# Kernel tuning notes

Measured on AMD Instinct MI355X. Metric: run time of the kernel, lower is better.

## Reference

```python
import jax, jax.numpy as jnp
import numpy as np

N = 50000      # nodes
E = 800000     # edges
G = 512        # graphs in batch
F0 = 92        # orig atom feature len
F = 64         # atom_fea_len
NB = 41        # nbr_fea_len
H = 128        # h_fea_len
NCONV = 3
EPS = 1e-5


def setup_inputs() -> dict:
    key = jax.random.key(0)
    ks = jax.random.split(key, 16)
    s = 0.05
    inp = {
        "x": jax.random.normal(ks[0], (N, F0), jnp.float32),
        "edge_index": jax.random.randint(ks[1], (2, E), 0, N),
        "edge_attr": jax.random.normal(ks[2], (E, NB), jnp.float32),
        "batch": jnp.sort(jax.random.randint(ks[3], (N,), 0, G)),
        # embedding (only applied at the first conv, when x width == F0)
        "emb_W": jax.random.normal(ks[4], (F0, F), jnp.float32) * s,
        "emb_b": jnp.zeros((F,), jnp.float32),
        # per-conv-layer params, stacked on leading axis
        "bn1_g": jnp.ones((NCONV, F), jnp.float32),
        "bn1_b": jnp.zeros((NCONV, F), jnp.float32),
        "bn2_g": jnp.ones((NCONV, F), jnp.float32),
        "bn2_b": jnp.zeros((NCONV, F), jnp.float32),
        "lnf_W": jax.random.normal(ks[5], (NCONV, 2 * F + NB, F), jnp.float32) * s,
        "lnf_b": jnp.zeros((NCONV, F), jnp.float32),
        "lns_W": jax.random.normal(ks[6], (NCONV, 2 * F + NB, F), jnp.float32) * s,
        "lns_b": jnp.zeros((NCONV, F), jnp.float32),
        # readout MLP
        "fc1_W": jax.random.normal(ks[7], (F, H), jnp.float32) * s,
        "fc1_b": jnp.zeros((H,), jnp.float32),
        "out_W": jax.random.normal(ks[8], (H, 1), jnp.float32) * s,
        "out_b": jnp.zeros((1,), jnp.float32),
    }
    return inp


def _batchnorm(x, g, b):
    # training-mode BatchNorm1d: batch stats over node dim, biased variance
    mean = jnp.mean(x, axis=0)
    var = jnp.var(x, axis=0)
    return (x - mean) * jax.lax.rsqrt(var + EPS) * g + b


def _cgconv(x, edge_index, edge_attr, bn1_g, bn1_b, bn2_g, bn2_b, Wf, bf, Ws, bs):
    x = _batchnorm(x, bn1_g, bn1_b)
    # flow='target_to_source': x_i = x[edge_index[0]], x_j = x[edge_index[1]],
    # aggregation scatter-adds messages to edge_index[0]
    src, dst = edge_index[0], edge_index[1]
    z = jnp.concatenate([x[src], x[dst], edge_attr], axis=-1)   # [E, 2F+NB]
    m = jax.nn.sigmoid(z @ Wf + bf) * jax.nn.softplus(z @ Ws + bs)
    agg = jax.ops.segment_sum(m, src, num_segments=x.shape[0])  # [N, F]
    out = _batchnorm(agg, bn2_g, bn2_b) + x
    return jax.nn.softplus(out)


def reference(x, edge_index, edge_attr, batch, emb_W, emb_b,
              bn1_g, bn1_b, bn2_g, bn2_b, lnf_W, lnf_b, lns_W, lns_b,
              fc1_W, fc1_b, out_W, out_b):
    h = x @ emb_W + emb_b  # first conv applies embedding (x width == F0)
    for i in range(NCONV):
        h = _cgconv(h, edge_index, edge_attr,
                    bn1_g[i], bn1_b[i], bn2_g[i], bn2_b[i],
                    lnf_W[i], lnf_b[i], lns_W[i], lns_b[i])
    # global mean pool per graph
    sums = jax.ops.segment_sum(h, batch, num_segments=G)
    cnts = jax.ops.segment_sum(jnp.ones((h.shape[0], 1), h.dtype), batch, num_segments=G)
    crys = sums / jnp.maximum(cnts, 1.0)                         # [G, F]
    crys = jax.nn.softplus(jax.nn.softplus(crys) @ fc1_W + fc1_b)
    return crys @ out_W + out_b                                  # [G, 1]
```

## Files before the change

### kernel.cpp

```cpp
#include <hip/hip_runtime.h>
#include <hip/hip_bf16.h>

#define NN 50000
#define NE 800000
#define NG 512
#define F0 92
#define FF 64
#define NB 41
#define HH 128
#define NBLK_SCAN 196
#define NBATCH (NE / 64)
#define WBSZ (2 * 8 * 64 * 8)

typedef __attribute__((ext_vector_type(4))) float f32x4;
typedef __attribute__((ext_vector_type(8))) short bf16x8;

__device__ __forceinline__ float softplusf(float x) {
    return fmaxf(x, 0.f) + __logf(1.f + __expf(-fabsf(x)));
}
__device__ __forceinline__ float sigmoidf(float x) {
    return __fdividef(1.f, 1.f + __expf(-x));
}
__device__ __forceinline__ ushort f2bf(float v) {
    __hip_bfloat16 b = __float2bfloat16(v);
    return *reinterpret_cast<ushort*>(&b);
}


__global__ __launch_bounds__(256) void hist_kernel(const int* __restrict__ ei,
                                                   int* __restrict__ cnt)
{
    for (int e = blockIdx.x * 256 + threadIdx.x; e < NE; e += gridDim.x * 256)
        atomicAdd(&cnt[ei[e]], 1);
}

__global__ __launch_bounds__(256) void scan1_kernel(const int* __restrict__ cnt,
                                                    int* __restrict__ bsum)
{
    __shared__ int sd[256];
    const int t = threadIdx.x;
    const int idx = blockIdx.x * 256 + t;
    sd[t] = (idx < NN) ? cnt[idx] : 0;
    __syncthreads();
    for (int s = 128; s > 0; s >>= 1) {
        if (t < s) sd[t] += sd[t + s];
        __syncthreads();
    }
    if (t == 0) bsum[blockIdx.x] = sd[0];
}

__global__ __launch_bounds__(256) void scan2_kernel(int* __restrict__ bsum)
{
    __shared__ int sd[256];
    const int t = threadIdx.x;
    const int v = (t < NBLK_SCAN) ? bsum[t] : 0;
    sd[t] = v;
    __syncthreads();
    for (int off = 1; off < 256; off <<= 1) {
        int a = (t >= off) ? sd[t - off] : 0;
        __syncthreads();
        sd[t] += a;
        __syncthreads();
    }
    if (t < NBLK_SCAN) bsum[t] = sd[t] - v;
}

__global__ __launch_bounds__(256) void scan3_kernel(const int* __restrict__ cnt,
                                                    const int* __restrict__ bsum,
                                                    int* __restrict__ cursor)
{
    __shared__ int sd[256];
    const int t = threadIdx.x;
    const int idx = blockIdx.x * 256 + t;
    const int v = (idx < NN) ? cnt[idx] : 0;
    sd[t] = v;
    __syncthreads();
    for (int off = 1; off < 256; off <<= 1) {
        int a = (t >= off) ? sd[t - off] : 0;
        __syncthreads();
        sd[t] += a;
        __syncthreads();
    }
    if (idx < NN) cursor[idx] = bsum[blockIdx.x] + sd[t] - v;
}

__global__ __launch_bounds__(256) void scatter_kernel(const int* __restrict__ ei,
                                                      int* __restrict__ cursor,
                                                      int4* __restrict__ esd)
{
    for (int e = blockIdx.x * 256 + threadIdx.x; e < NE; e += gridDim.x * 256) {
        const int s = ei[e];
        const int d = ei[NE + e];
        const int pos = atomicAdd(&cursor[s], 1);
        esd[pos] = make_int4(e, s, d, 0);
    }
}

__global__ __launch_bounds__(256) void pack_kernel(const float* __restrict__ ea,
                                                   const int4* __restrict__ esd,
                                                   ushort* __restrict__ eaP)
{
    const int pos = blockIdx.x * 256 + threadIdx.x;
    if (pos >= NE) return;
    const int e = esd[pos].x;
    const float* row = ea + (size_t)e * NB;
    const int gg = pos >> 4, rw = pos & 15;
#pragma unroll
    for (int t2 = 0; t2 < 2; ++t2)
#pragma unroll
        for (int lg = 0; lg < 4; ++lg) {
            ushort buf[8] __attribute__((aligned(16)));
#pragma unroll
            for (int j = 0; j < 8; ++j) {
                const int k = t2 * 32 + lg * 8 + j;
                buf[j] = (k < NB) ? f2bf(row[k]) : (ushort)0;
            }
            *(int4*)&eaP[(((size_t)gg * 2 + t2) * 64 + lg * 16 + rw) * 8] =
                *(const int4*)buf;
        }
}

__global__ __launch_bounds__(256) void prep_kernel(
    const float* __restrict__ lnfW, const float* __restrict__ lnsW,
    ushort* __restrict__ wB)
{
    const int total = 3 * WBSZ;
    for (int idx = blockIdx.x * 256 + threadIdx.x; idx < total; idx += gridDim.x * 256) {
        const int j = idx & 7;
        const int lane = (idx >> 3) & 63;
        const int nt = (idx >> 9) & 7;
        const int t2 = (idx >> 12) & 1;
        const int i = idx >> 13;
        const int k = t2 * 32 + (lane >> 4) * 8 + j;
        const int col = (nt & 3) * 16 + (lane & 15);
        const float* W = (nt < 4 ? lnfW : lnsW) + (size_t)i * 169 * FF;
        wB[idx] = (k < NB) ? f2bf(W[(2 * FF + k) * FF + col]) : (ushort)0;
    }
}


__global__ __launch_bounds__(256) void emb_kernel(
    const float* __restrict__ x, const float* __restrict__ W,
    const float* __restrict__ bias, float* __restrict__ h,
    float* __restrict__ stats0)
{
    __shared__ float sx[4][F0];
    __shared__ float sdr[2][4][FF];
    const int lane = threadIdx.x & 63;
    const int w = threadIdx.x >> 6;
    float wr[F0];
#pragma unroll
    for (int k = 0; k < F0; ++k) wr[k] = W[k * FF + lane];
    const float bv = bias[lane];
    float s = 0.f, s2 = 0.f;
    const int nit = NN / 4;
    for (int it = blockIdx.x; it < nit; it += gridDim.x) {
        const int n = it * 4 + w;
        if (lane < 46) {
            sx[w][lane * 2]     = x[n * F0 + lane * 2];
            sx[w][lane * 2 + 1] = x[n * F0 + lane * 2 + 1];
        }
        __syncthreads();
        float acc = bv;
#pragma unroll
        for (int k4 = 0; k4 < F0 / 4; ++k4) {
            float4 q = *(const float4*)&sx[w][k4 * 4];
            acc = fmaf(q.x, wr[k4 * 4 + 0], acc);
            acc = fmaf(q.y, wr[k4 * 4 + 1], acc);
            acc = fmaf(q.z, wr[k4 * 4 + 2], acc);
            acc = fmaf(q.w, wr[k4 * 4 + 3], acc);
        }
        h[n * FF + lane] = acc;
        s += acc;
        s2 = fmaf(acc, acc, s2);
        __syncthreads();
    }
    sdr[0][w][lane] = s;
    sdr[1][w][lane] = s2;
    __syncthreads();
    if (threadIdx.x < FF) {
        const int f = threadIdx.x;
        atomicAdd(&stats0[f],      sdr[0][0][f] + sdr[0][1][f] + sdr[0][2][f] + sdr[0][3][f]);
        atomicAdd(&stats0[FF + f], sdr[1][0][f] + sdr[1][1][f] + sdr[1][2][f] + sdr[1][3][f]);
    }
}

__global__ __launch_bounds__(256) void stats_kernel(
    const float* __restrict__ src, float* __restrict__ stats)
{
    __shared__ float sd[2][4][FF];
    const int f = threadIdx.x & 63;
    const int r = threadIdx.x >> 6;
    float s = 0.f, s2 = 0.f;
    for (int n = blockIdx.x * 4 + r; n < NN; n += gridDim.x * 4) {
        float v = src[n * FF + f];
        s += v;
        s2 = fmaf(v, v, s2);
    }
    sd[0][r][f] = s;
    sd[1][r][f] = s2;
    __syncthreads();
    if (threadIdx.x < FF) {
        atomicAdd(&stats[f],      sd[0][0][f] + sd[0][1][f] + sd[0][2][f] + sd[0][3][f]);
        atomicAdd(&stats[FF + f], sd[1][0][f] + sd[1][1][f] + sd[1][2][f] + sd[1][3][f]);
    }
}

__global__ void finalize_kernel(const float* __restrict__ g, const float* __restrict__ b,
                                float* __restrict__ stats)
{
    const int f = threadIdx.x;
    const float inv = 1.f / (float)NN;
    float mean = stats[f] * inv;
    float var = stats[FF + f] * inv - mean * mean;
    float rstd = rsqrtf(var + 1e-5f);
    float A = rstd * g[f];
    stats[2 * FF + f] = A;
    stats[3 * FF + f] = fmaf(-mean, A, b[f]);
}

__global__ __launch_bounds__(256) void node_kernel(
    const float* __restrict__ h, const float* __restrict__ stats,
    const float* __restrict__ Wf, const float* __restrict__ Ws,
    const float* __restrict__ bf, const float* __restrict__ bs,
    float* __restrict__ xn, float* __restrict__ pS, float* __restrict__ pD)
{
    __shared__ float sx[4][FF];
    const int lane = threadIdx.x & 63;
    const int w = threadIdx.x >> 6;
    const float* W = (w < 2) ? Wf : Ws;
    const int rowbase = (w & 1) * FF;
    float wr[FF];
#pragma unroll
    for (int k = 0; k < FF; ++k) wr[k] = W[(rowbase + k) * FF + lane];
    const float A = stats[2 * FF + lane];
    const float B = stats[3 * FF + lane];
    float bias = 0.f;
    if (w == 0) bias = bf[lane];
    if (w == 2) bias = bs[lane];
    float* outp = ((w & 1) ? pD : pS) + ((w >> 1) & 1);
    for (int n = blockIdx.x; n < NN; n += gridDim.x) {
        const float xv = fmaf(h[n * FF + lane], A, B);
        if (w == 0) xn[n * FF + lane] = xv;
        sx[w][lane] = xv;
        __syncthreads();
        float acc = bias;
#pragma unroll
        for (int k4 = 0; k4 < FF / 4; ++k4) {
            float4 q = *(const float4*)&sx[w][k4 * 4];
            acc = fmaf(q.x, wr[k4 * 4 + 0], acc);
            acc = fmaf(q.y, wr[k4 * 4 + 1], acc);
            acc = fmaf(q.z, wr[k4 * 4 + 2], acc);
            acc = fmaf(q.w, wr[k4 * 4 + 3], acc);
        }
        outp[(size_t)n * 128 + 2 * lane] = acc;
        __syncthreads();
    }
}

__global__ __launch_bounds__(256) __attribute__((amdgpu_waves_per_eu(4, 4)))
void edge_kernel(const ushort* __restrict__ eaP, const int4* __restrict__ esd,
                 const ushort* __restrict__ wB,
                 const float* __restrict__ pS, const float* __restrict__ pD,
                 float* __restrict__ agg)
{
    __shared__ ushort wlds[WBSZ];
    __shared__ float  mld[4][64 * 17 + 4];
    __shared__ int    sld[4][64];
    __shared__ int    dld[4][64];
    const int t = threadIdx.x, lane = t & 63, w = t >> 6;
    for (int i = t; i < WBSZ / 8; i += 256)
        ((int4*)wlds)[i] = ((const int4*)wB)[i];
    __syncthreads();
    const int le = lane >> 4, lf = lane & 15;
    const int nw = (gridDim.x * 256) >> 6;
    const int gw = (blockIdx.x * 256 + t) >> 6;

    for (int b = gw; b < NBATCH; b += nw) {
        const int pos = b * 64 + lane;
        const int4 rec = esd[pos];
        sld[w][lane] = rec.y;
        dld[w][lane] = rec.z;
        bf16x8 af[4][2];
#pragma unroll
        for (int g = 0; g < 4; ++g)
#pragma unroll
            for (int t2 = 0; t2 < 2; ++t2)
                af[g][t2] = *(const bf16x8*)&eaP[(((size_t)(b * 4 + g) * 2 + t2) * 64 + lane) * 8];

#pragma unroll
        for (int p = 0; p < 4; ++p) {
            const bf16x8 bG0 = *(const bf16x8*)&wlds[((0 * 8 + p) * 64 + lane) * 8];
            const bf16x8 bG1 = *(const bf16x8*)&wlds[((1 * 8 + p) * 64 + lane) * 8];
            const bf16x8 bC0 = *(const bf16x8*)&wlds[((0 * 8 + p + 4) * 64 + lane) * 8];
            const bf16x8 bC1 = *(const bf16x8*)&wlds[((1 * 8 + p + 4) * 64 + lane) * 8];
            const int f = p * 16 + lf;
#pragma unroll
            for (int g = 0; g < 4; ++g) {
                f32x4 aG = {0.f, 0.f, 0.f, 0.f}, aC = {0.f, 0.f, 0.f, 0.f};
                aG = __builtin_amdgcn_mfma_f32_16x16x32_bf16(af[g][0], bG0, aG, 0, 0, 0);
                aG = __builtin_amdgcn_mfma_f32_16x16x32_bf16(af[g][1], bG1, aG, 0, 0, 0);
                aC = __builtin_amdgcn_mfma_f32_16x16x32_bf16(af[g][0], bC0, aC, 0, 0, 0);
                aC = __builtin_amdgcn_mfma_f32_16x16x32_bf16(af[g][1], bC1, aC, 0, 0, 0);
                const int eb = g * 16 + le * 4;
#pragma unroll
                for (int r = 0; r < 4; ++r) {
                    const int eidx = eb + r;
                    const int sv = sld[w][eidx];
                    const int dv = dld[w][eidx];
                    const float2 s2 = *(const float2*)(pS + (size_t)sv * 128 + 2 * f);
                    const float2 d2 = *(const float2*)(pD + (size_t)dv * 128 + 2 * f);
                    mld[w][eidx * 17 + lf] =
                        sigmoidf(aG[r] + s2.x + d2.x) * softplusf(aC[r] + s2.y + d2.y);
                }
            }
            const int f0 = p * 16;
            for (int s = 0; s < 16; ++s) {
                const int eidx = s * 4 + le;
                float v = mld[w][eidx * 17 + lf];
                const int sA = sld[w][eidx];
                const int sB = (le <= 2) ? sld[w][eidx + 1] : -1;
                const int sC = (le <= 1) ? sld[w][eidx + 2] : -1;
                const float t1 = __shfl_down(v, 16, 64);
                if (sB == sA) v += t1;
                const float t2v = __shfl_down(v, 32, 64);
                if (sC == sA) v += t2v;
                const bool head = (le == 0) || (sld[w][eidx - 1] != sA);
                if (head) unsafeAtomicAdd(&agg[(size_t)sA * FF + f0 + lf], v);
            }
        }
    }
}

__global__ __launch_bounds__(256) void update_kernel(
    const float* __restrict__ agg, const float* __restrict__ xn,
    const float* __restrict__ stats, float* __restrict__ h,
    const int* __restrict__ batch, float* __restrict__ pool,
    float* __restrict__ pcnt, float* __restrict__ statsNext, const int do_pool)
{
    __shared__ float sdr[2][4][FF];
    float s = 0.f, s2 = 0.f;
    const int total = NN * FF;
    for (int idx = blockIdx.x * blockDim.x + threadIdx.x; idx < total;
         idx += gridDim.x * blockDim.x) {
        const int f = idx & 63;
        const int n = idx >> 6;
        const float A = stats[2 * FF + f];
        const float B = stats[3 * FF + f];
        const float v = softplusf(fmaf(agg[idx], A, B) + xn[idx]);
        if (do_pool) {
            const int g = batch[n];
            unsafeAtomicAdd(&pool[g * FF + f], v);
            if (f == 0) unsafeAtomicAdd(&pcnt[g], 1.f);
        } else {
            h[idx] = v;
            s += v;
            s2 = fmaf(v, v, s2);
        }
    }
    if (!do_pool) {
        const int f = threadIdx.x & 63, r = threadIdx.x >> 6;
        sdr[0][r][f] = s;
        sdr[1][r][f] = s2;
        __syncthreads();
        if (threadIdx.x < FF) {
            atomicAdd(&statsNext[f],      sdr[0][0][f] + sdr[0][1][f] + sdr[0][2][f] + sdr[0][3][f]);
            atomicAdd(&statsNext[FF + f], sdr[1][0][f] + sdr[1][1][f] + sdr[1][2][f] + sdr[1][3][f]);
        }
    }
}

__global__ __launch_bounds__(128) void readout_kernel(
    const float* __restrict__ pool, const float* __restrict__ pcnt,
    const float* __restrict__ fc1W, const float* __restrict__ fc1b,
    const float* __restrict__ outW, const float* __restrict__ outb,
    float* __restrict__ out)
{
    __shared__ float sp[FF];
    __shared__ float red[2];
    const int g = blockIdx.x;
    const int t = threadIdx.x;
    if (t < FF) {
        const float c = fmaxf(pcnt[g], 1.f);
        sp[t] = softplusf(pool[g * FF + t] / c);
    }
    __syncthreads();
    float a = fc1b[t];
#pragma unroll
    for (int k = 0; k < FF; ++k) a = fmaf(sp[k], fc1W[k * HH + t], a);
    float o = softplusf(a) * outW[t];
#pragma unroll
    for (int off = 32; off > 0; off >>= 1) o += __shfl_down(o, off, 64);
    if ((t & 63) == 0) red[t >> 6] = o;
    __syncthreads();
    if (t == 0) out[g] = red[0] + red[1] + outb[0];
}

extern "C" void kernel_launch(void* const* d_in, const int* in_sizes, int n_in,
                              void* d_out, int out_size, void* d_ws, size_t ws_size,
                              hipStream_t stream)
{
    const float* x     = (const float*)d_in[0];
    const int*   ei    = (const int*)  d_in[1];
    const float* ea    = (const float*)d_in[2];
    const int*   batch = (const int*)  d_in[3];
    const float* embW  = (const float*)d_in[4];
    const float* embb  = (const float*)d_in[5];
    const float* bn1g  = (const float*)d_in[6];
    const float* bn1b  = (const float*)d_in[7];
    const float* bn2g  = (const float*)d_in[8];
    const float* bn2b  = (const float*)d_in[9];
    const float* lnfW  = (const float*)d_in[10];
    const float* lnfb  = (const float*)d_in[11];
    const float* lnsW  = (const float*)d_in[12];
    const float* lnsb  = (const float*)d_in[13];
    const float* fc1W  = (const float*)d_in[14];
    const float* fc1b  = (const float*)d_in[15];
    const float* outW  = (const float*)d_in[16];
    const float* outb  = (const float*)d_in[17];

    float* ws      = (float*)d_ws;
    float* h       = ws;
    float* xn      = h   + (size_t)NN * FF;
    float* pS      = xn  + (size_t)NN * FF;
    float* pD      = pS  + (size_t)NN * 128;
    float* agg     = pD  + (size_t)NN * 128;
    float* pool    = agg + (size_t)NN * FF;
    float* pcnt    = pool + (size_t)NG * FF;
    float* statsB1 = pcnt + NG;
    float* statsB2 = statsB1 + 3 * 256;
    int*   cnt     = (int*)(statsB2 + 3 * 256);
    int*   cursor  = cnt + NN;
    int*   bsum    = cursor + NN;
    int4*  esd     = (int4*)(bsum + 256);
    ushort* wB     = (ushort*)(esd + NE);
    ushort* eaP    = wB + 3 * WBSZ;

    hipMemsetAsync(cnt, 0, NN * sizeof(int), stream);
    hipMemsetAsync(pool, 0, (NG * FF + NG + 6 * 256) * sizeof(float), stream);

    hist_kernel<<<2048, 256, 0, stream>>>(ei, cnt);
    scan1_kernel<<<NBLK_SCAN, 256, 0, stream>>>(cnt, bsum);
    scan2_kernel<<<1, 256, 0, stream>>>(bsum);
    scan3_kernel<<<NBLK_SCAN, 256, 0, stream>>>(cnt, bsum, cursor);
    scatter_kernel<<<2048, 256, 0, stream>>>(ei, cursor, esd);
    pack_kernel<<<(NE + 255) / 256, 256, 0, stream>>>(ea, esd, eaP);
    prep_kernel<<<96, 256, 0, stream>>>(lnfW, lnsW, wB);
    emb_kernel<<<1024, 256, 0, stream>>>(x, embW, embb, h, statsB1);

    for (int i = 0; i < 3; ++i) {
        const float* Wf  = lnfW + (size_t)i * 169 * FF;
        const float* Wsp = lnsW + (size_t)i * 169 * FF;
        float* s1 = statsB1 + (size_t)i * 256;
        float* s2 = statsB2 + (size_t)i * 256;
        finalize_kernel<<<1, 64, 0, stream>>>(bn1g + i * FF, bn1b + i * FF, s1);
        node_kernel<<<1024, 256, 0, stream>>>(h, s1, Wf, Wsp,
                                              lnfb + i * FF, lnsb + i * FF, xn, pS, pD);
        hipMemsetAsync(agg, 0, (size_t)NN * FF * sizeof(float), stream);
        edge_kernel<<<1024, 256, 0, stream>>>(eaP, esd, wB + (size_t)i * WBSZ,
                                              pS, pD, agg);
        stats_kernel<<<256, 256, 0, stream>>>(agg, s2);
        finalize_kernel<<<1, 64, 0, stream>>>(bn2g + i * FF, bn2b + i * FF, s2);
        update_kernel<<<2048, 256, 0, stream>>>(agg, xn, s2, h, batch, pool, pcnt,
                                                statsB1 + (size_t)(i + 1 < 3 ? i + 1 : 0) * 256,
                                                (i == 2) ? 1 : 0);
    }
    readout_kernel<<<NG, HH, 0, stream>>>(pool, pcnt, fc1W, fc1b, outW, outb, (float*)d_out);
}
```

Before: 948.6 us.

## Pack edge features in original order, gather per edge in edge kernel, fold BN finalize

The pack kernel now converts edge attributes to bf16 in original edge order, staging rows through shared memory, so it no longer does a sorted-order indirect gather. The edge kernel instead gathers each edge's packed row by its original id, obtained with lane shuffles. It also drops the LDS staging of messages and the segmented reduction, replacing them with a per-lane running sum over 4 consecutive sorted edges and atomics at segment breaks. The BN finalize kernels are folded into node_kernel and update_kernel, and the edge grid is doubled with the waves_per_eu hint removed. The trade-offs are random gathers of edge features, more global atomics per edge, and unroll-1 loops that may limit latency hiding.

After: 1.057 ms. 1.11x slower.

```diff
diff --git a/kernel.cpp b/kernel.cpp
--- a/kernel.cpp
+++ b/kernel.cpp
@@ -11,6 +11,7 @@
 #define NBLK_SCAN 196
 #define NBATCH (NE / 64)
 #define WBSZ (2 * 8 * 64 * 8)
+#define PACK_EB 128
 
 typedef __attribute__((ext_vector_type(4))) float f32x4;
 typedef __attribute__((ext_vector_type(8))) short bf16x8;
@@ -96,28 +97,24 @@
     }
 }
 
-__global__ __launch_bounds__(256) void pack_kernel(const float* __restrict__ ea,
-                                                   const int4* __restrict__ esd,
+__global__ __launch_bounds__(128) void pack_kernel(const float* __restrict__ ea,
                                                    ushort* __restrict__ eaP)
 {
-    const int pos = blockIdx.x * 256 + threadIdx.x;
-    if (pos >= NE) return;
-    const int e = esd[pos].x;
-    const float* row = ea + (size_t)e * NB;
-    const int gg = pos >> 4, rw = pos & 15;
-#pragma unroll
-    for (int t2 = 0; t2 < 2; ++t2)
-#pragma unroll
-        for (int lg = 0; lg < 4; ++lg) {
-            ushort buf[8] __attribute__((aligned(16)));
-#pragma unroll
-            for (int j = 0; j < 8; ++j) {
-                const int k = t2 * 32 + lg * 8 + j;
-                buf[j] = (k < NB) ? f2bf(row[k]) : (ushort)0;
-            }
-            *(int4*)&eaP[(((size_t)gg * 2 + t2) * 64 + lg * 16 + rw) * 8] =
-                *(const int4*)buf;
-        }
+    __shared__ float rowbuf[PACK_EB * NB];
+    const int t = threadIdx.x;
+    const size_t base = (size_t)blockIdx.x * PACK_EB;
+    const float* src = ea + base * NB;
+    for (int i = t; i < PACK_EB * NB; i += 128) rowbuf[i] = src[i];
+    __syncthreads();
+    uint* out = (uint*)eaP + base * 32;
+#pragma unroll
+    for (int i = 0; i < 32; ++i) {
+        const int idx = i * 128 + t;
+        const int e = idx >> 5, k2 = (idx & 31) * 2;
+        const float v0 = (k2 < NB) ? rowbuf[e * NB + k2] : 0.f;
+        const float v1 = (k2 + 1 < NB) ? rowbuf[e * NB + k2 + 1] : 0.f;
+        out[idx] = (uint)f2bf(v0) | ((uint)f2bf(v1) << 16);
+    }
 }
 
 __global__ __launch_bounds__(256) void prep_kernel(
@@ -206,21 +203,9 @@
     }
 }
 
-__global__ void finalize_kernel(const float* __restrict__ g, const float* __restrict__ b,
-                                float* __restrict__ stats)
-{
-    const int f = threadIdx.x;
-    const float inv = 1.f / (float)NN;
-    float mean = stats[f] * inv;
-    float var = stats[FF + f] * inv - mean * mean;
-    float rstd = rsqrtf(var + 1e-5f);
-    float A = rstd * g[f];
-    stats[2 * FF + f] = A;
-    stats[3 * FF + f] = fmaf(-mean, A, b[f]);
-}
-
 __global__ __launch_bounds__(256) void node_kernel(
     const float* __restrict__ h, const float* __restrict__ stats,
+    const float* __restrict__ gbn, const float* __restrict__ bbn,
     const float* __restrict__ Wf, const float* __restrict__ Ws,
     const float* __restrict__ bf, const float* __restrict__ bs,
     float* __restrict__ xn, float* __restrict__ pS, float* __restrict__ pD)
@@ -233,8 +218,11 @@
     float wr[FF];
 #pragma unroll
     for (int k = 0; k < FF; ++k) wr[k] = W[(rowbase + k) * FF + lane];
-    const float A = stats[2 * FF + lane];
-    const float B = stats[3 * FF + lane];
+    const float inv = 1.f / (float)NN;
+    const float mean = stats[lane] * inv;
+    const float var = stats[FF + lane] * inv - mean * mean;
+    const float A = rsqrtf(var + 1e-5f) * gbn[lane];
+    const float B = fmaf(-mean, A, bbn[lane]);
     float bias = 0.f;
     if (w == 0) bias = bf[lane];
     if (w == 2) bias = bs[lane];
@@ -258,17 +246,14 @@
     }
 }
 
-__global__ __launch_bounds__(256) __attribute__((amdgpu_waves_per_eu(4, 4)))
+__global__ __launch_bounds__(256)
 void edge_kernel(const ushort* __restrict__ eaP, const int4* __restrict__ esd,
                  const ushort* __restrict__ wB,
                  const float* __restrict__ pS, const float* __restrict__ pD,
                  float* __restrict__ agg)
 {
     __shared__ ushort wlds[WBSZ];
-    __shared__ float  mld[4][64 * 17 + 4];
-    __shared__ int    sld[4][64];
-    __shared__ int    dld[4][64];
-    const int t = threadIdx.x, lane = t & 63, w = t >> 6;
+    const int t = threadIdx.x, lane = t & 63;
     for (int i = t; i < WBSZ / 8; i += 256)
         ((int4*)wlds)[i] = ((const int4*)wB)[i];
     __syncthreads();
@@ -277,56 +262,53 @@
     const int gw = (blockIdx.x * 256 + t) >> 6;
 
     for (int b = gw; b < NBATCH; b += nw) {
-        const int pos = b * 64 + lane;
-        const int4 rec = esd[pos];
-        sld[w][lane] = rec.y;
-        dld[w][lane] = rec.z;
-        bf16x8 af[4][2];
-#pragma unroll
-        for (int g = 0; g < 4; ++g)
-#pragma unroll
-            for (int t2 = 0; t2 < 2; ++t2)
-                af[g][t2] = *(const bf16x8*)&eaP[(((size_t)(b * 4 + g) * 2 + t2) * 64 + lane) * 8];
-
-#pragma unroll
-        for (int p = 0; p < 4; ++p) {
-            const bf16x8 bG0 = *(const bf16x8*)&wlds[((0 * 8 + p) * 64 + lane) * 8];
-            const bf16x8 bG1 = *(const bf16x8*)&wlds[((1 * 8 + p) * 64 + lane) * 8];
-            const bf16x8 bC0 = *(const bf16x8*)&wlds[((0 * 8 + p + 4) * 64 + lane) * 8];
-            const bf16x8 bC1 = *(const bf16x8*)&wlds[((1 * 8 + p + 4) * 64 + lane) * 8];
-            const int f = p * 16 + lf;
-#pragma unroll
-            for (int g = 0; g < 4; ++g) {
+        const int4 rec = esd[b * 64 + lane];
+#pragma unroll 1
+        for (int g = 0; g < 4; ++g) {
+            const int eg  = __shfl(rec.x, g * 16 + lf, 64);
+            const int sv0 = __shfl(rec.y, g * 16 + le * 4 + 0, 64);
+            const int sv1 = __shfl(rec.y, g * 16 + le * 4 + 1, 64);
+            const int sv2 = __shfl(rec.y, g * 16 + le * 4 + 2, 64);
+            const int sv3 = __shfl(rec.y, g * 16 + le * 4 + 3, 64);
+            const int dv0 = __shfl(rec.z, g * 16 + le * 4 + 0, 64);
+            const int dv1 = __shfl(rec.z, g * 16 + le * 4 + 1, 64);
+            const int dv2 = __shfl(rec.z, g * 16 + le * 4 + 2, 64);
+            const int dv3 = __shfl(rec.z, g * 16 + le * 4 + 3, 64);
+            const bf16x8 af0 = *(const bf16x8*)&eaP[(size_t)eg * 64 + le * 8];
+            const bf16x8 af1 = *(const bf16x8*)&eaP[(size_t)eg * 64 + 32 + le * 8];
+#pragma unroll 1
+            for (int p = 0; p < 4; ++p) {
+                const bf16x8 bG0 = *(const bf16x8*)&wlds[((0 * 8 + p) * 64 + lane) * 8];
+                const bf16x8 bG1 = *(const bf16x8*)&wlds[((1 * 8 + p) * 64 + lane) * 8];
+                const bf16x8 bC0 = *(const bf16x8*)&wlds[((0 * 8 + p + 4) * 64 + lane) * 8];
+                const bf16x8 bC1 = *(const bf16x8*)&wlds[((1 * 8 + p + 4) * 64 + lane) * 8];
                 f32x4 aG = {0.f, 0.f, 0.f, 0.f}, aC = {0.f, 0.f, 0.f, 0.f};
-                aG = __builtin_amdgcn_mfma_f32_16x16x32_bf16(af[g][0], bG0, aG, 0, 0, 0);
-                aG = __builtin_amdgcn_mfma_f32_16x16x32_bf16(af[g][1], bG1, aG, 0, 0, 0);
-                aC = __builtin_amdgcn_mfma_f32_16x16x32_bf16(af[g][0], bC0, aC, 0, 0, 0);
-                aC = __builtin_amdgcn_mfma_f32_16x16x32_bf16(af[g][1], bC1, aC, 0, 0, 0);
-                const int eb = g * 16 + le * 4;
-#pragma unroll
-                for (int r = 0; r < 4; ++r) {
-                    const int eidx = eb + r;
-                    const int sv = sld[w][eidx];
-                    const int dv = dld[w][eidx];
-                    const float2 s2 = *(const float2*)(pS + (size_t)sv * 128 + 2 * f);
-                    const float2 d2 = *(const float2*)(pD + (size_t)dv * 128 + 2 * f);
-                    mld[w][eidx * 17 + lf] =
-                        sigmoidf(aG[r] + s2.x + d2.x) * softplusf(aC[r] + s2.y + d2.y);
-                }
-            }
-            const int f0 = p * 16;
-            for (int s = 0; s < 16; ++s) {
-                const int eidx = s * 4 + le;
-                float v = mld[w][eidx * 17 + lf];
-                const int sA = sld[w][eidx];
-                const int sB = (le <= 2) ? sld[w][eidx + 1] : -1;
-                const int sC = (le <= 1) ? sld[w][eidx + 2] : -1;
-                const float t1 = __shfl_down(v, 16, 64);
-                if (sB == sA) v += t1;
-                const float t2v = __shfl_down(v, 32, 64);
-                if (sC == sA) v += t2v;
-                const bool head = (le == 0) || (sld[w][eidx - 1] != sA);
-                if (head) unsafeAtomicAdd(&agg[(size_t)sA * FF + f0 + lf], v);
+                aG = __builtin_amdgcn_mfma_f32_16x16x32_bf16(af0, bG0, aG, 0, 0, 0);
+                aG = __builtin_amdgcn_mfma_f32_16x16x32_bf16(af1, bG1, aG, 0, 0, 0);
+                aC = __builtin_amdgcn_mfma_f32_16x16x32_bf16(af0, bC0, aC, 0, 0, 0);
+                aC = __builtin_amdgcn_mfma_f32_16x16x32_bf16(af1, bC1, aC, 0, 0, 0);
+                const int fo = 2 * (p * 16 + lf);
+                const float2 s20 = *(const float2*)(pS + (size_t)sv0 * 128 + fo);
+                const float2 d20 = *(const float2*)(pD + (size_t)dv0 * 128 + fo);
+                const float2 s21 = *(const float2*)(pS + (size_t)sv1 * 128 + fo);
+                const float2 d21 = *(const float2*)(pD + (size_t)dv1 * 128 + fo);
+                const float2 s22 = *(const float2*)(pS + (size_t)sv2 * 128 + fo);
+                const float2 d22 = *(const float2*)(pD + (size_t)dv2 * 128 + fo);
+                const float2 s23 = *(const float2*)(pS + (size_t)sv3 * 128 + fo);
+                const float2 d23 = *(const float2*)(pD + (size_t)dv3 * 128 + fo);
+                const float m0 = sigmoidf(aG[0] + s20.x + d20.x) * softplusf(aC[0] + s20.y + d20.y);
+                const float m1 = sigmoidf(aG[1] + s21.x + d21.x) * softplusf(aC[1] + s21.y + d21.y);
+                const float m2 = sigmoidf(aG[2] + s22.x + d22.x) * softplusf(aC[2] + s22.y + d22.y);
+                const float m3 = sigmoidf(aG[3] + s23.x + d23.x) * softplusf(aC[3] + s23.y + d23.y);
+                const int fcol = p * 16 + lf;
+                float run = m0;
+                if (sv1 == sv0) run += m1;
+                else { unsafeAtomicAdd(&agg[(size_t)sv0 * FF + fcol], run); run = m1; }
+                if (sv2 == sv1) run += m2;
+                else { unsafeAtomicAdd(&agg[(size_t)sv1 * FF + fcol], run); run = m2; }
+                if (sv3 == sv2) run += m3;
+                else { unsafeAtomicAdd(&agg[(size_t)sv2 * FF + fcol], run); run = m3; }
+                unsafeAtomicAdd(&agg[(size_t)sv3 * FF + fcol], run);
             }
         }
     }
@@ -334,24 +316,29 @@
 
 __global__ __launch_bounds__(256) void update_kernel(
     const float* __restrict__ agg, const float* __restrict__ xn,
-    const float* __restrict__ stats, float* __restrict__ h,
-    const int* __restrict__ batch, float* __restrict__ pool,
-    float* __restrict__ pcnt, float* __restrict__ statsNext, const int do_pool)
+    const float* __restrict__ stats,
+    const float* __restrict__ gbn, const float* __restrict__ bbn,
+    float* __restrict__ h, const int* __restrict__ batch,
+    float* __restrict__ pool, float* __restrict__ pcnt,
+    float* __restrict__ statsNext, const int do_pool)
 {
     __shared__ float sdr[2][4][FF];
+    const int myf = threadIdx.x & 63;
+    const float inv = 1.f / (float)NN;
+    const float mean = stats[myf] * inv;
+    const float var = stats[FF + myf] * inv - mean * mean;
+    const float A = rsqrtf(var + 1e-5f) * gbn[myf];
+    const float B = fmaf(-mean, A, bbn[myf]);
     float s = 0.f, s2 = 0.f;
     const int total = NN * FF;
     for (int idx = blockIdx.x * blockDim.x + threadIdx.x; idx < total;
          idx += gridDim.x * blockDim.x) {
-        const int f = idx & 63;
         const int n = idx >> 6;
-        const float A = stats[2 * FF + f];
-        const float B = stats[3 * FF + f];
         const float v = softplusf(fmaf(agg[idx], A, B) + xn[idx]);
         if (do_pool) {
             const int g = batch[n];
-            unsafeAtomicAdd(&pool[g * FF + f], v);
-            if (f == 0) unsafeAtomicAdd(&pcnt[g], 1.f);
+            unsafeAtomicAdd(&pool[g * FF + myf], v);
+            if (myf == 0) unsafeAtomicAdd(&pcnt[g], 1.f);
         } else {
             h[idx] = v;
             s += v;
@@ -359,13 +346,13 @@
         }
     }
     if (!do_pool) {
-        const int f = threadIdx.x & 63, r = threadIdx.x >> 6;
-        sdr[0][r][f] = s;
-        sdr[1][r][f] = s2;
+        const int r = threadIdx.x >> 6;
+        sdr[0][r][myf] = s;
+        sdr[1][r][myf] = s2;
         __syncthreads();
         if (threadIdx.x < FF) {
-            atomicAdd(&statsNext[f],      sdr[0][0][f] + sdr[0][1][f] + sdr[0][2][f] + sdr[0][3][f]);
-            atomicAdd(&statsNext[FF + f], sdr[1][0][f] + sdr[1][1][f] + sdr[1][2][f] + sdr[1][3][f]);
+            atomicAdd(&statsNext[myf],      sdr[0][0][myf] + sdr[0][1][myf] + sdr[0][2][myf] + sdr[0][3][myf]);
+            atomicAdd(&statsNext[FF + myf], sdr[1][0][myf] + sdr[1][1][myf] + sdr[1][2][myf] + sdr[1][3][myf]);
         }
     }
 }
@@ -444,7 +431,7 @@
     scan2_kernel<<<1, 256, 0, stream>>>(bsum);
     scan3_kernel<<<NBLK_SCAN, 256, 0, stream>>>(cnt, bsum, cursor);
     scatter_kernel<<<2048, 256, 0, stream>>>(ei, cursor, esd);
-    pack_kernel<<<(NE + 255) / 256, 256, 0, stream>>>(ea, esd, eaP);
+    pack_kernel<<<NE / PACK_EB, 128, 0, stream>>>(ea, eaP);
     prep_kernel<<<96, 256, 0, stream>>>(lnfW, lnsW, wB);
     emb_kernel<<<1024, 256, 0, stream>>>(x, embW, embb, h, statsB1);
 
@@ -453,15 +440,15 @@
         const float* Wsp = lnsW + (size_t)i * 169 * FF;
         float* s1 = statsB1 + (size_t)i * 256;
         float* s2 = statsB2 + (size_t)i * 256;
-        finalize_kernel<<<1, 64, 0, stream>>>(bn1g + i * FF, bn1b + i * FF, s1);
-        node_kernel<<<1024, 256, 0, stream>>>(h, s1, Wf, Wsp,
-                                              lnfb + i * FF, lnsb + i * FF, xn, pS, pD);
+        node_kernel<<<1024, 256, 0, stream>>>(h, s1, bn1g + i * FF, bn1b + i * FF,
+                                              Wf, Wsp, lnfb + i * FF, lnsb + i * FF,
+                                              xn, pS, pD);
         hipMemsetAsync(agg, 0, (size_t)NN * FF * sizeof(float), stream);
-        edge_kernel<<<1024, 256, 0, stream>>>(eaP, esd, wB + (size_t)i * WBSZ,
+        edge_kernel<<<2048, 256, 0, stream>>>(eaP, esd, wB + (size_t)i * WBSZ,
                                               pS, pD, agg);
         stats_kernel<<<256, 256, 0, stream>>>(agg, s2);
-        finalize_kernel<<<1, 64, 0, stream>>>(bn2g + i * FF, bn2b + i * FF, s2);
-        update_kernel<<<2048, 256, 0, stream>>>(agg, xn, s2, h, batch, pool, pcnt,
+        update_kernel<<<2048, 256, 0, stream>>>(agg, xn, s2, bn2g + i * FF, bn2b + i * FF,
+                                                h, batch, pool, pcnt,
                                                 statsB1 + (size_t)(i + 1 < 3 ? i + 1 : 0) * 256,
                                                 (i == 2) ? 1 : 0);
     }
```
